# Optimization experiments

Measured on AMD Instinct MI355X. Metric: run time of the kernel, lower is better.

The kernel has to match this reference:

```python
import jax, jax.numpy as jnp
import numpy as np

B, N, F, E, H, A, V, L = 128, 196, 512, 512, 512, 512, 30000, 21


def setup_inputs() -> dict:
    key = jax.random.key(0)
    ks = jax.random.split(key, 20)
    s = 0.02
    d = {
        "feats": jax.random.normal(ks[0], (B, N, F), jnp.float32),
        "captions": jax.random.randint(ks[1], (B, L), 1, V),
        "embed_W": (jax.random.normal(ks[2], (V, E), jnp.float32) * s).at[0].set(0.0),
        "Wf_w": jax.random.normal(ks[3], (A, F), jnp.float32) * s,
        "Wf_b": jnp.zeros((A,), jnp.float32),
        "Wh_w": jax.random.normal(ks[4], (A, H), jnp.float32) * s,
        "Wh_b": jnp.zeros((A,), jnp.float32),
        "v_w": jax.random.normal(ks[5], (1, A), jnp.float32) * s,
        "v_b": jnp.zeros((1,), jnp.float32),
        "W_ih": jax.random.normal(ks[6], (4 * H, E + F), jnp.float32) * s,
        "W_hh": jax.random.normal(ks[7], (4 * H, H), jnp.float32) * s,
        "b_ih": jnp.zeros((4 * H,), jnp.float32),
        "b_hh": jnp.zeros((4 * H,), jnp.float32),
        "init_w": jax.random.normal(ks[8], (H, F), jnp.float32) * s,
        "init_b": jnp.zeros((H,), jnp.float32),
        "initc_w": jax.random.normal(ks[9], (H, F), jnp.float32) * s,
        "initc_b": jnp.zeros((H,), jnp.float32),
        "out_w": jax.random.normal(ks[10], (V, H), jnp.float32) * s,
        "out_b": jnp.zeros((V,), jnp.float32),
    }
    return d


def reference(feats, captions, embed_W, Wf_w, Wf_b, Wh_w, Wh_b, v_w, v_b,
              W_ih, W_hh, b_ih, b_hh, init_w, init_b, initc_w, initc_b,
              out_w, out_b):
    # padding_idx=0 -> embedding row 0 is zero
    emW = embed_W.at[0].set(0.0)
    emb = emW[captions[:, :-1]]                       # [B, T, E], T = L-1
    gfeat = feats.mean(axis=1)                        # [B, F]
    h0 = gfeat @ init_w.T + init_b                    # [B, H]
    c0 = gfeat @ initc_w.T + initc_b                  # [B, H]
    # attention feature projection is timestep-invariant: hoist out of loop
    fproj = jnp.einsum('bnf,af->bna', feats, Wf_w) + Wf_b  # [B, N, A]

    def step(carry, emb_t):
        h, c = carry
        hproj = h @ Wh_w.T + Wh_b                     # [B, A]
        e = jnp.tanh(fproj + hproj[:, None, :])       # [B, N, A]
        scores = jnp.einsum('bna,a->bn', e, v_w[0]) + v_b[0]
        w = jax.nn.softmax(scores, axis=1)            # [B, N]
        ctx = jnp.einsum('bnf,bn->bf', feats, w)      # [B, F]
        x = jnp.concatenate([emb_t, ctx], axis=1)     # [B, E+F]
        gates = x @ W_ih.T + b_ih + h @ W_hh.T + b_hh # [B, 4H]
        i, f, g, o = jnp.split(gates, 4, axis=1)      # torch gate order i,f,g,o
        i = jax.nn.sigmoid(i)
        f = jax.nn.sigmoid(f)
        g = jnp.tanh(g)
        o = jax.nn.sigmoid(o)
        c = f * c + i * g
        h = o * jnp.tanh(c)
        logit = h @ out_w.T + out_b                   # [B, V]
        return (h, c), logit

    _, logits = jax.lax.scan(step, (h0, c0), jnp.swapaxes(emb, 0, 1))
    return jnp.swapaxes(logits, 0, 1)                 # [B, T, V]
```

## Files before the change

kernel.cpp:

```cpp
#include <hip/hip_runtime.h>
#include <stdint.h>
#include <stddef.h>

typedef unsigned short u16;
typedef __attribute__((ext_vector_type(8))) short short8;
typedef __attribute__((ext_vector_type(4))) float f32x4;

#define DEV static __device__ __forceinline__

DEV float bf2f(u16 u){ return __uint_as_float(((unsigned)u)<<16); }
DEV u16 f2bf(float f){ unsigned x=__float_as_uint(f); return (u16)((x + 0x7fffu + ((x>>16)&1u))>>16); }

DEV float wsum(float v){
#pragma unroll
  for(int o=32;o;o>>=1) v += __shfl_xor(v,o);
  return v;
}
DEV float wmax(float v){
#pragma unroll
  for(int o=32;o;o>>=1) v = fmaxf(v,__shfl_xor(v,o));
  return v;
}
DEV float sigm(float x){ return __fdividef(1.f, 1.f+__expf(-x)); }
DEV float tanhx(float x){ float e=__expf(-2.f*fabsf(x)); float t=__fdividef(1.f-e,1.f+e); return x<0.f?-t:t; }

DEV f32x4 mfma16(short8 a, short8 b, f32x4 c){
  asm("v_mfma_f32_16x16x32_bf16 %0, %1, %2, %0" : "+v"(c) : "v"(a), "v"(b));
  return c;
}
DEV void gll16(const void* g, void* l){
  __builtin_amdgcn_global_load_lds((const __attribute__((address_space(1))) void*)g,
                                   (__attribute__((address_space(3))) void*)l, 16, 0, 0);
}

DEV void pack8(u16* dst, const float* src){
  const float4 a=*(const float4*)(src);
  const float4 b=*(const float4*)(src+4);
  short8 o;
  o[0]=(short)f2bf(a.x); o[1]=(short)f2bf(a.y); o[2]=(short)f2bf(a.z); o[3]=(short)f2bf(a.w);
  o[4]=(short)f2bf(b.x); o[5]=(short)f2bf(b.y); o[6]=(short)f2bf(b.z); o[7]=(short)f2bf(b.w);
  *(short8*)dst=o;
}
DEV void zero8(u16* dst){
  short8 z;
#pragma unroll
  for(int e=0;e<8;++e) z[e]=0;
  *(short8*)dst=z;
}

__global__ __launch_bounds__(256) void setup_cast(
  const float* __restrict__ feats, const int* __restrict__ captions,
  const float* __restrict__ embW, const float* __restrict__ Wf_w,
  const float* __restrict__ Wh_w, const float* __restrict__ W_ih,
  const float* __restrict__ W_hh, const float* __restrict__ b_ih,
  const float* __restrict__ b_hh, const float* __restrict__ out_w,
  u16* __restrict__ feats_bf, u16* __restrict__ outw_bf, u16* __restrict__ Wc,
  u16* __restrict__ WihE, u16* __restrict__ embx, u16* __restrict__ Whw_bf,
  u16* __restrict__ Wf_bf, float* __restrict__ bias_comb)
{
  const long long o0=12845056LL,o1=28246016LL,o2=30343168LL,o3=31391744LL,
                  o4=32702464LL,o5=32964608LL,o6=33226752LL,total=33228800LL;
  for (long long i8=((long long)blockIdx.x*256+threadIdx.x)*8; i8<total;
       i8+=(long long)gridDim.x*256*8){
    const long long i=i8;
    if (i<o0){ pack8(feats_bf+i, feats+i); }
    else if (i<o1){ const long long j=i-o0; const int r=(int)(j>>9);
      if (r<30000) pack8(outw_bf+j, out_w+j); else zero8(outw_bf+j); }
    else if (i<o2){ const long long j=i-o1; const int r=(int)(j>>10), k=(int)(j&1023);
      const int o=((r&3)<<9)+(r>>2);
      const float* s=(k<512)? (W_ih+(size_t)o*1024+512+k) : (W_hh+(size_t)o*512+(k-512));
      pack8(Wc+j, s); }
    else if (i<o3){ const long long j=i-o2; const int r=(int)(j>>9), k=(int)(j&511);
      const int o=((r&3)<<9)+(r>>2);
      pack8(WihE+j, W_ih+(size_t)o*1024+k); }
    else if (i<o4){ const long long j=i-o3; const int m=(int)(j>>9), e=(int)(j&511);
      const int b=m/20, tt=m-b*20; const int idx=captions[b*21+tt];
      if (idx) pack8(embx+j, embW+(size_t)idx*512+e); else zero8(embx+j); }
    else if (i<o5){ const long long j=i-o4; pack8(Whw_bf+j, Wh_w+j); }
    else if (i<o6){ const long long j=i-o5; pack8(Wf_bf+j, Wf_w+j); }
    else { const long long j=i-o6;
      for(int e=0;e<8;++e){ const int r=(int)(j+e); const int o=((r&3)<<9)+(r>>2);
        bias_comb[r]=b_ih[o]+b_hh[o]; } }
  }
}

__global__ __launch_bounds__(256) void prep(
  const float* __restrict__ feats, const float* __restrict__ init_w,
  const float* __restrict__ init_b, const float* __restrict__ initc_w,
  const float* __restrict__ initc_b, u16* __restrict__ xs0, float* __restrict__ cbuf)
{
  const int b=blockIdx.x, tid=threadIdx.x, lane=tid&63, w=tid>>6;
  __shared__ float gf[512];
  const float* fb=feats+(size_t)b*196*512;
  float a0=0.f,a1=0.f;
  for(int n=0;n<196;++n){ a0+=fb[(size_t)n*512+tid]; a1+=fb[(size_t)n*512+tid+256]; }
  gf[tid]=a0*(1.f/196.f); gf[tid+256]=a1*(1.f/196.f);
  __syncthreads();
  const int kb=lane*8;
  float g8[8];
#pragma unroll
  for(int e=0;e<8;++e) g8[e]=gf[kb+e];
  for(int j=w*128;j<w*128+128;++j){
    const float* r1=init_w+(size_t)j*512+kb;
    const float* r2=initc_w+(size_t)j*512+kb;
    float s1=0.f,s2=0.f;
#pragma unroll
    for(int e=0;e<8;++e){ s1+=g8[e]*r1[e]; s2+=g8[e]*r2[e]; }
    s1=wsum(s1); s2=wsum(s2);
    if(lane==(j&63)){ xs0[b*1024+512+j]=f2bf(s1+init_b[j]); cbuf[b*512+j]=s2+initc_b[j]; }
  }
}

__global__ __launch_bounds__(1024) void attn_step(
  const u16* __restrict__ fproj, const u16* __restrict__ feats_bf,
  u16* __restrict__ xs, const u16* __restrict__ Whw,
  const float* __restrict__ Whb, const float* __restrict__ vw,
  const float* __restrict__ vb, const float* __restrict__ gemb,
  const float* __restrict__ gpart, float* __restrict__ cbuf,
  u16* __restrict__ h_all, int t)
{
  const int b=blockIdx.x, tid=threadIdx.x, lane=tid&63, w=tid>>6;
  __shared__ float part[16][512];
  __shared__ float hsf[512], hp[512], sc[208], red[16];
  if (t>0){
    if (tid<512){
      const int u=tid;
      float4 g4=*(const float4*)&gemb[((size_t)b*20+(t-1))*2048+u*4];
#pragma unroll
      for(int kz=0;kz<4;++kz){
        const float4 p=*(const float4*)&gpart[((size_t)kz*128+b)*2048+u*4];
        g4.x+=p.x; g4.y+=p.y; g4.z+=p.z; g4.w+=p.w;
      }
      const float cn=sigm(g4.y)*cbuf[b*512+u]+sigm(g4.x)*tanhx(g4.z);
      const float hn=sigm(g4.w)*tanhx(cn);
      cbuf[b*512+u]=cn;
      const u16 hb=f2bf(hn);
      xs[b*1024+512+u]=hb;
      h_all[((size_t)b*20+(t-1))*512+u]=hb;
      hsf[u]=bf2f(hb);
    }
  } else {
    if (tid<512) hsf[tid]=bf2f(xs[b*1024+512+tid]);
  }
  __syncthreads();
  const int kb=lane*8;
  float h8[8];
#pragma unroll
  for(int e=0;e<8;++e) h8[e]=hsf[kb+e];
  for(int jj=0;jj<32;jj+=2){
    const int j=w*32+jj;
    short8 w0=*(const short8*)(Whw+(size_t)j*512+kb);
    short8 w1=*(const short8*)(Whw+(size_t)(j+1)*512+kb);
    float s0=0.f,s1=0.f;
#pragma unroll
    for(int e=0;e<8;++e){
      s0+=h8[e]*bf2f((u16)w0[e]);
      s1+=h8[e]*bf2f((u16)w1[e]);
    }
    s0=wsum(s0); s1=wsum(s1);
    if(lane==0){ hp[j]=s0+Whb[j]; hp[j+1]=s1+Whb[j+1]; }
  }
  __syncthreads();
  float p2[8], vm2[8];
  float sv=0.f;
#pragma unroll
  for(int e=0;e<8;++e){
    const float p=hp[kb+e], v=vw[kb+e];
    p2[e]=2.f*p; vm2[e]=-2.f*v; sv+=v;
  }
  const float vb0=vb[0];
#pragma unroll
  for(int i=0;i<12;i+=2){
    const int n0=w+16*i, n1=n0+16;
    short8 f0=*(const short8*)(fproj+((size_t)b*196+n0)*512+kb);
    short8 f1=*(const short8*)(fproj+((size_t)b*196+n1)*512+kb);
    float s0=sv, s1=sv;
#pragma unroll
    for(int e=0;e<8;++e){
      const float x0=fmaf(bf2f((u16)f0[e]),2.f,p2[e]);
      const float x1=fmaf(bf2f((u16)f1[e]),2.f,p2[e]);
      s0+=__fdividef(vm2[e],__expf(x0)+1.f);
      s1+=__fdividef(vm2[e],__expf(x1)+1.f);
    }
    s0=wsum(s0); s1=wsum(s1);
    if(lane==0){ sc[n0]=s0+vb0; sc[n1]=s1+vb0; }
  }
  {
    const int n=w+192;
    if (n<196){
      short8 f0=*(const short8*)(fproj+((size_t)b*196+n)*512+kb);
      float s0=sv;
#pragma unroll
      for(int e=0;e<8;++e){
        const float x0=fmaf(bf2f((u16)f0[e]),2.f,p2[e]);
        s0+=__fdividef(vm2[e],__expf(x0)+1.f);
      }
      s0=wsum(s0);
      if(lane==0) sc[n]=s0+vb0;
    }
  }
  __syncthreads();
  float xv=(tid<196)? sc[tid] : -3.0e38f;
  float mx=wmax(xv);
  if(lane==0) red[w]=mx;
  __syncthreads();
  float mm=red[0];
#pragma unroll
  for(int i=1;i<16;++i) mm=fmaxf(mm,red[i]);
  float pv=(tid<196)? __expf(xv-mm) : 0.f;
  float ps=wsum(pv);
  __syncthreads();
  if(lane==0) red[w]=ps;
  __syncthreads();
  float tot=red[0];
#pragma unroll
  for(int i=1;i<16;++i) tot+=red[i];
  if(tid<196) sc[tid]=__fdividef(pv,tot);
  __syncthreads();
  float a8[8];
#pragma unroll
  for(int e=0;e<8;++e) a8[e]=0.f;
  for(int n=w;n<196;n+=16){
    short8 fv=*(const short8*)(feats_bf+((size_t)b*196+n)*512+kb);
    const float wn=sc[n];
#pragma unroll
    for(int e=0;e<8;++e) a8[e]+=wn*bf2f((u16)fv[e]);
  }
  *(float4*)&part[w][kb]  =*(float4*)&a8[0];
  *(float4*)&part[w][kb+4]=*(float4*)&a8[4];
  __syncthreads();
  if (tid<512){
    float s=0.f;
#pragma unroll
    for(int i=0;i<16;++i) s+=part[i][tid];
    xs[b*1024+tid]=f2bf(s);
  }
}

__global__ __launch_bounds__(512) void lstm_fin(
  const float* __restrict__ gemb, const float* __restrict__ gpart,
  const float* __restrict__ cbuf, u16* __restrict__ h_all)
{
  const int b=blockIdx.x, u=threadIdx.x;
  float4 g4=*(const float4*)&gemb[((size_t)b*20+19)*2048+u*4];
#pragma unroll
  for(int kz=0;kz<4;++kz){
    const float4 p=*(const float4*)&gpart[((size_t)kz*128+b)*2048+u*4];
    g4.x+=p.x; g4.y+=p.y; g4.z+=p.z; g4.w+=p.w;
  }
  const float cn=sigm(g4.y)*cbuf[b*512+u]+sigm(g4.x)*tanhx(g4.z);
  const float hn=sigm(g4.w)*tanhx(cn);
  h_all[((size_t)b*20+19)*512+u]=f2bf(hn);
}

template<int MODE>
__global__ __launch_bounds__(256) void gemm_bt(
  const u16* __restrict__ A, int lda, const u16* __restrict__ Bw, int ldb, int K,
  const float* __restrict__ bias, float* __restrict__ outf, u16* __restrict__ outb,
  int ncols)
{
  const int bm=(MODE==4)? 0 : blockIdx.y*128;
  const int kz=(MODE==4)? blockIdx.y : 0;
  const int bn=blockIdx.x*128;
  const u16* __restrict__ Ap=A +(size_t)kz*256;
  const u16* __restrict__ Bp=Bw+(size_t)kz*256;
  const int tid=threadIdx.x, lane=tid&63, wave=tid>>6;
  const int wr=(wave>>1)*64, wc=(wave&1)*64;
  __shared__ u16 As[128*32], Bs[128*32];
  f32x4 acc[4][4]={};
  const int srow=tid>>2, scol=(tid&3)*8;
  for(int k0=0;k0<K;k0+=32){
    gll16(Ap+(size_t)(bm+srow)*lda    +k0+scol, As+tid*8);
    gll16(Ap+(size_t)(bm+64+srow)*lda +k0+scol, As+2048+tid*8);
    gll16(Bp+(size_t)(bn+srow)*ldb    +k0+scol, Bs+tid*8);
    gll16(Bp+(size_t)(bn+64+srow)*ldb +k0+scol, Bs+2048+tid*8);
    __syncthreads();
    short8 af[4], bfr[4];
    const int ro=lane&15, ko=(lane>>4)*8;
#pragma unroll
    for(int m=0;m<4;++m) af[m]=*(const short8*)(As+(wr+m*16+ro)*32+ko);
#pragma unroll
    for(int n=0;n<4;++n) bfr[n]=*(const short8*)(Bs+(wc+n*16+ro)*32+ko);
#pragma unroll
    for(int m=0;m<4;++m)
#pragma unroll
      for(int n=0;n<4;++n) acc[m][n]=mfma16(af[m],bfr[n],acc[m][n]);
    __syncthreads();
  }
  asm volatile("s_nop 7\ns_nop 7\ns_nop 7");
  const int ro4=(lane>>4)*4, co=lane&15;
#pragma unroll
  for(int m=0;m<4;++m)
#pragma unroll
    for(int n=0;n<4;++n)
#pragma unroll
      for(int j=0;j<4;++j){
        const int r=bm+wr+m*16+ro4+j, c=bn+wc+n*16+co;
        if constexpr (MODE==0)      outb[(size_t)r*ncols+c]=f2bf(acc[m][n][j]+bias[c]);
        else if constexpr (MODE==1) outf[(size_t)r*ncols+c]=acc[m][n][j]+bias[c];
        else if constexpr (MODE==2){ if (c<ncols) outf[(size_t)r*ncols+c]=acc[m][n][j]+bias[c]; }
        else                        outf[((size_t)kz*128+r)*ncols+c]=acc[m][n][j];
      }
}

extern "C" void kernel_launch(void* const* d_in, const int* in_sizes, int n_in,
                              void* d_out, int out_size, void* d_ws, size_t ws_size,
                              hipStream_t stream) {
  const float* feats   =(const float*)d_in[0];
  const int*   captions=(const int*)  d_in[1];
  const float* embW    =(const float*)d_in[2];
  const float* Wf_w    =(const float*)d_in[3];
  const float* Wf_b    =(const float*)d_in[4];
  const float* Wh_w    =(const float*)d_in[5];
  const float* Wh_b    =(const float*)d_in[6];
  const float* v_w     =(const float*)d_in[7];
  const float* v_b     =(const float*)d_in[8];
  const float* W_ih    =(const float*)d_in[9];
  const float* W_hh    =(const float*)d_in[10];
  const float* b_ih    =(const float*)d_in[11];
  const float* b_hh    =(const float*)d_in[12];
  const float* init_w  =(const float*)d_in[13];
  const float* init_b  =(const float*)d_in[14];
  const float* initc_w =(const float*)d_in[15];
  const float* initc_b =(const float*)d_in[16];
  const float* out_w   =(const float*)d_in[17];
  const float* out_b   =(const float*)d_in[18];
  float* out=(float*)d_out;
  char* ws=(char*)d_ws;

  u16*   feats_bf =(u16*)  (ws+0);
  u16*   fproj    =(u16*)  (ws+25690112);
  u16*   outw_bf  =(u16*)  (ws+51380224);
  u16*   Wc       =(u16*)  (ws+82182144);
  u16*   WihE     =(u16*)  (ws+86376448);
  u16*   Whw_bf   =(u16*)  (ws+88473600);
  u16*   Wf_bf    =(u16*)  (ws+88997888);
  u16*   embx     =(u16*)  (ws+89522176);
  u16*   h_all    =(u16*)  (ws+92143616);
  u16*   xs0      =(u16*)  (ws+94765056);
  float* gemb     =(float*)(ws+95289344);
  float* cbuf     =(float*)(ws+116260864);
  float* bias_comb=(float*)(ws+116523008);
  float* gpart    =(float*)(ws+116531200);

  setup_cast<<<4096,256,0,stream>>>(feats,captions,embW,Wf_w,Wh_w,W_ih,W_hh,b_ih,b_hh,out_w,
                                    feats_bf,outw_bf,Wc,WihE,embx,Whw_bf,Wf_bf,bias_comb);
  prep<<<128,256,0,stream>>>(feats,init_w,init_b,initc_w,initc_b,xs0,cbuf);
  gemm_bt<0><<<dim3(4,196),256,0,stream>>>(feats_bf,512,Wf_bf,512,512,
      Wf_b,nullptr,fproj,512);
  gemm_bt<1><<<dim3(16,20),256,0,stream>>>(embx,512,WihE,512,512,
      bias_comb,gemb,nullptr,2048);

  for(int t=0;t<20;++t){
    attn_step<<<128,1024,0,stream>>>(fproj,feats_bf,xs0,Whw_bf,Wh_b,v_w,v_b,
                                     gemb,gpart,cbuf,h_all,t);
    gemm_bt<4><<<dim3(16,4),256,0,stream>>>(xs0,1024,Wc,1024,256,
        nullptr,gpart,nullptr,2048);
  }
  lstm_fin<<<128,512,0,stream>>>(gemb,gpart,cbuf,h_all);
  gemm_bt<2><<<dim3(235,20),256,0,stream>>>(h_all,512,outw_bf,512,512,
      out_b,out,nullptr,30000);
}
```

Measured before the change: 1.245 ms.

## Unroll attention loops by four and swap output GEMM grid order

The per-step attention kernel now processes four rows per iteration in the Wh projection, the score computation and the context accumulation, so more independent global loads and wave reductions are in flight. The context loop is unrolled with a separate tail. The final vocab GEMM swaps its grid axes so consecutive blocks share the same out_w column tile, which should improve L2 reuse of the large weight matrix. Workspace offsets for bias_comb and gpart are also moved. The wider unroll raises register pressure in the 1024-thread attention kernel.

```diff
diff --git a/kernel.cpp b/kernel.cpp
--- a/kernel.cpp
+++ b/kernel.cpp
@@ -147,18 +147,25 @@
   float h8[8];
 #pragma unroll
   for(int e=0;e<8;++e) h8[e]=hsf[kb+e];
-  for(int jj=0;jj<32;jj+=2){
+#pragma unroll
+  for(int jj=0;jj<32;jj+=4){
     const int j=w*32+jj;
     short8 w0=*(const short8*)(Whw+(size_t)j*512+kb);
     short8 w1=*(const short8*)(Whw+(size_t)(j+1)*512+kb);
-    float s0=0.f,s1=0.f;
+    short8 w2=*(const short8*)(Whw+(size_t)(j+2)*512+kb);
+    short8 w3=*(const short8*)(Whw+(size_t)(j+3)*512+kb);
+    float s0=0.f,s1=0.f,s2=0.f,s3=0.f;
 #pragma unroll
     for(int e=0;e<8;++e){
-      s0+=h8[e]*bf2f((u16)w0[e]);
-      s1+=h8[e]*bf2f((u16)w1[e]);
-    }
-    s0=wsum(s0); s1=wsum(s1);
-    if(lane==0){ hp[j]=s0+Whb[j]; hp[j+1]=s1+Whb[j+1]; }
+      const float he=h8[e];
+      s0+=he*bf2f((u16)w0[e]);
+      s1+=he*bf2f((u16)w1[e]);
+      s2+=he*bf2f((u16)w2[e]);
+      s3+=he*bf2f((u16)w3[e]);
+    }
+    s0=wsum(s0); s1=wsum(s1); s2=wsum(s2); s3=wsum(s3);
+    if(lane==0){ hp[j]=s0+Whb[j]; hp[j+1]=s1+Whb[j+1];
+                 hp[j+2]=s2+Whb[j+2]; hp[j+3]=s3+Whb[j+3]; }
   }
   __syncthreads();
   float p2[8], vm2[8];
@@ -170,20 +177,27 @@
   }
   const float vb0=vb[0];
 #pragma unroll
-  for(int i=0;i<12;i+=2){
-    const int n0=w+16*i, n1=n0+16;
-    short8 f0=*(const short8*)(fproj+((size_t)b*196+n0)*512+kb);
-    short8 f1=*(const short8*)(fproj+((size_t)b*196+n1)*512+kb);
-    float s0=sv, s1=sv;
+  for(int i=0;i<12;i+=4){
+    const int n0=w+16*i;
+    short8 f0=*(const short8*)(fproj+((size_t)b*196+n0   )*512+kb);
+    short8 f1=*(const short8*)(fproj+((size_t)b*196+n0+16)*512+kb);
+    short8 f2=*(const short8*)(fproj+((size_t)b*196+n0+32)*512+kb);
+    short8 f3=*(const short8*)(fproj+((size_t)b*196+n0+48)*512+kb);
+    float s0=sv,s1=sv,s2=sv,s3=sv;
 #pragma unroll
     for(int e=0;e<8;++e){
-      const float x0=fmaf(bf2f((u16)f0[e]),2.f,p2[e]);
-      const float x1=fmaf(bf2f((u16)f1[e]),2.f,p2[e]);
-      s0+=__fdividef(vm2[e],__expf(x0)+1.f);
-      s1+=__fdividef(vm2[e],__expf(x1)+1.f);
-    }
-    s0=wsum(s0); s1=wsum(s1);
-    if(lane==0){ sc[n0]=s0+vb0; sc[n1]=s1+vb0; }
+      s0+=__fdividef(vm2[e],__expf(fmaf(bf2f((u16)f0[e]),2.f,p2[e]))+1.f);
+      s1+=__fdividef(vm2[e],__expf(fmaf(bf2f((u16)f1[e]),2.f,p2[e]))+1.f);
+      s2+=__fdividef(vm2[e],__expf(fmaf(bf2f((u16)f2[e]),2.f,p2[e]))+1.f);
+      s3+=__fdividef(vm2[e],__expf(fmaf(bf2f((u16)f3[e]),2.f,p2[e]))+1.f);
+    }
+    s0=wsum(s0); s1=wsum(s1); s2=wsum(s2); s3=wsum(s3);
+    if(lane==0){
+      sc[n0   ]=s0+vb0;
+      sc[n0+16]=s1+vb0;
+      sc[n0+32]=s2+vb0;
+      sc[n0+48]=s3+vb0;
+    }
   }
   {
     const int n=w+192;
@@ -191,10 +205,8 @@
       short8 f0=*(const short8*)(fproj+((size_t)b*196+n)*512+kb);
       float s0=sv;
 #pragma unroll
-      for(int e=0;e<8;++e){
-        const float x0=fmaf(bf2f((u16)f0[e]),2.f,p2[e]);
-        s0+=__fdividef(vm2[e],__expf(x0)+1.f);
-      }
+      for(int e=0;e<8;++e)
+        s0+=__fdividef(vm2[e],__expf(fmaf(bf2f((u16)f0[e]),2.f,p2[e]))+1.f);
       s0=wsum(s0);
       if(lane==0) sc[n]=s0+vb0;
     }
@@ -220,11 +232,27 @@
   float a8[8];
 #pragma unroll
   for(int e=0;e<8;++e) a8[e]=0.f;
-  for(int n=w;n<196;n+=16){
-    short8 fv=*(const short8*)(feats_bf+((size_t)b*196+n)*512+kb);
-    const float wn=sc[n];
-#pragma unroll
-    for(int e=0;e<8;++e) a8[e]+=wn*bf2f((u16)fv[e]);
+#pragma unroll
+  for(int i=0;i<12;i+=4){
+    const int n0=w+16*i;
+    short8 v0=*(const short8*)(feats_bf+((size_t)b*196+n0   )*512+kb);
+    short8 v1=*(const short8*)(feats_bf+((size_t)b*196+n0+16)*512+kb);
+    short8 v2=*(const short8*)(feats_bf+((size_t)b*196+n0+32)*512+kb);
+    short8 v3=*(const short8*)(feats_bf+((size_t)b*196+n0+48)*512+kb);
+    const float wn0=sc[n0], wn1=sc[n0+16], wn2=sc[n0+32], wn3=sc[n0+48];
+#pragma unroll
+    for(int e=0;e<8;++e)
+      a8[e]+=wn0*bf2f((u16)v0[e])+wn1*bf2f((u16)v1[e])
+            +wn2*bf2f((u16)v2[e])+wn3*bf2f((u16)v3[e]);
+  }
+  {
+    const int n=w+192;
+    if (n<196){
+      short8 v0=*(const short8*)(feats_bf+((size_t)b*196+n)*512+kb);
+      const float wn=sc[n];
+#pragma unroll
+      for(int e=0;e<8;++e) a8[e]+=wn*bf2f((u16)v0[e]);
+    }
   }
   *(float4*)&part[w][kb]  =*(float4*)&a8[0];
   *(float4*)&part[w][kb+4]=*(float4*)&a8[4];
@@ -259,9 +287,9 @@
   const float* __restrict__ bias, float* __restrict__ outf, u16* __restrict__ outb,
   int ncols)
 {
-  const int bm=(MODE==4)? 0 : blockIdx.y*128;
+  const int bm=(MODE==4)? 0 : ((MODE==2)? blockIdx.x*128 : blockIdx.y*128);
+  const int bn=(MODE==2)? blockIdx.y*128 : blockIdx.x*128;
   const int kz=(MODE==4)? blockIdx.y : 0;
-  const int bn=blockIdx.x*128;
   const u16* __restrict__ Ap=A +(size_t)kz*256;
   const u16* __restrict__ Bp=Bw+(size_t)kz*256;
   const int tid=threadIdx.x, lane=tid&63, wave=tid>>6;
@@ -340,8 +368,8 @@
   u16*   xs0      =(u16*)  (ws+94765056);
   float* gemb     =(float*)(ws+95289344);
   float* cbuf     =(float*)(ws+116260864);
-  float* bias_comb=(float*)(ws+116523008);
-  float* gpart    =(float*)(ws+116531200);
+  float* bias_comb=(float*)(ws+116785152);
+  float* gpart    =(float*)(ws+116793344);
 
   setup_cast<<<4096,256,0,stream>>>(feats,captions,embW,Wf_w,Wh_w,W_ih,W_hh,b_ih,b_hh,out_w,
                                     feats_bf,outw_bf,Wc,WihE,embx,Whw_bf,Wf_bf,bias_comb);
@@ -358,6 +386,6 @@
         nullptr,gpart,nullptr,2048);
   }
   lstm_fin<<<128,512,0,stream>>>(gemb,gpart,cbuf,h_all);
-  gemm_bt<2><<<dim3(235,20),256,0,stream>>>(h_all,512,outw_bf,512,512,
+  gemm_bt<2><<<dim3(20,235),256,0,stream>>>(h_all,512,outw_bf,512,512,
       out_b,out,nullptr,30000);
 }
```

Result: faster. 1.172 ms (-5.9%).
